# Kernel tuning notes

Measured on AMD Instinct MI355X. Metric: run time of the kernel, lower is better.

The kernel has to match this reference:

```python
import jax, jax.numpy as jnp
import numpy as np
import math

D_MODEL, D_K, D_V, H = 512, 64, 64, 8

def setup_inputs() -> dict:
    key = jax.random.key(0)
    ks = jax.random.split(key, 8)
    B, L = 2, 4096
    q = jax.random.normal(ks[0], (B, L, D_MODEL), dtype=jnp.float32)
    k = jax.random.normal(ks[1], (B, L, D_MODEL), dtype=jnp.float32)
    v = jax.random.normal(ks[2], (B, L, D_MODEL), dtype=jnp.float32)
    attention_mask = jnp.ones((B, L), dtype=jnp.int32)
    s = 1.0 / math.sqrt(D_MODEL)
    Wq = jax.random.uniform(ks[3], (D_MODEL, H * D_K), dtype=jnp.float32, minval=-s, maxval=s)
    Wk = jax.random.uniform(ks[4], (D_MODEL, H * D_K), dtype=jnp.float32, minval=-s, maxval=s)
    Wv = jax.random.uniform(ks[5], (D_MODEL, H * D_V), dtype=jnp.float32, minval=-s, maxval=s)
    so = 1.0 / math.sqrt(H * D_V)
    Wo = jax.random.uniform(ks[6], (H * D_V, D_MODEL), dtype=jnp.float32, minval=-so, maxval=so)
    return {"q": q, "k": k, "v": v, "attention_mask": attention_mask,
            "Wq": Wq, "Wk": Wk, "Wv": Wv, "Wo": Wo}

def reference(q, k, v, attention_mask, Wq, Wk, Wv, Wo):
    B, L, _ = q.shape
    scale = 1.0 / math.sqrt(D_K)
    # project and split heads: [B, H, L, d]
    qh = (q @ Wq).reshape(B, L, H, D_K).transpose(0, 2, 1, 3)
    kh = (k @ Wk).reshape(B, L, H, D_K).transpose(0, 2, 1, 3)
    vh = (v @ Wv).reshape(B, L, H, D_V).transpose(0, 2, 1, 3)
    score = jnp.einsum('bhqd,bhkd->bhqk', qh, kh) * scale  # [B,H,L,L]
    mask = attention_mask[:, None, None, :]  # [B,1,1,L]
    score = jnp.where(mask == 0, -jnp.inf, score)
    attn = jax.nn.softmax(score, axis=-1)
    out = jnp.einsum('bhqk,bhkd->bhqd', attn, vh)
    out = out.transpose(0, 2, 1, 3).reshape(B, L, H * D_V)
    return out @ Wo
```

## Files before the change

kernel.cpp:

```cpp
#include <hip/hip_runtime.h>

typedef short bf16x8 __attribute__((ext_vector_type(8)));
typedef float f32x4 __attribute__((ext_vector_type(4)));
typedef unsigned short u16x8 __attribute__((ext_vector_type(8)));

static __device__ __forceinline__ unsigned short f2bf(float f) {
  unsigned int x = __builtin_bit_cast(unsigned int, f);
  x += 0x7FFFu + ((x >> 16) & 1u);
  return (unsigned short)(x >> 16);
}
static __device__ __forceinline__ unsigned int pk2bf(float a, float b) {
  unsigned int ia = __builtin_bit_cast(unsigned int, a) + 0x8000u;
  unsigned int ib = __builtin_bit_cast(unsigned int, b) + 0x8000u;
  return __builtin_amdgcn_perm(ib, ia, 0x07060302u);
}
static __device__ __forceinline__ void gl2lds16(const unsigned short* g, unsigned short* l) {
  __builtin_amdgcn_global_load_lds(
      (const __attribute__((address_space(1))) unsigned int*)g,
      (__attribute__((address_space(3))) unsigned int*)l, 16, 0, 0);
}

__global__ __launch_bounds__(256) void cvt3(const float* __restrict__ q, const float* __restrict__ k,
                                            const float* __restrict__ v,
                                            unsigned short* __restrict__ xbf) {
  const int sec = blockIdx.y;
  const float* src = (sec == 0) ? q : (sec == 1) ? k : v;
  int i = (blockIdx.x * 256 + threadIdx.x) * 8;
  int row = i >> 9, col = i & 511;
  float4 a = *(const float4*)(src + i);
  float4 b = *(const float4*)(src + i + 4);
  uint4 pk;
  pk.x = pk2bf(a.x, a.y); pk.y = pk2bf(a.z, a.w);
  pk.z = pk2bf(b.x, b.y); pk.w = pk2bf(b.z, b.w);
  *(uint4*)(xbf + (size_t)row * 1536 + sec * 512 + col) = pk;
}

__global__ __launch_bounds__(256) void wtrans4(const float* __restrict__ Wq, const float* __restrict__ Wk,
                                               const float* __restrict__ Wv, const float* __restrict__ Wo,
                                               unsigned short* __restrict__ WT) {
  __shared__ __align__(16) float T[64 * 68];
  const int z = blockIdx.z;
  const float* W = (z == 0) ? Wq : (z == 1) ? Wk : (z == 2) ? Wv : Wo;
  unsigned short* out = WT + (size_t)z * 512 * 512;
  const int k0 = blockIdx.x * 64, n0 = blockIdx.y * 64;
  const int tid = threadIdx.x;
#pragma unroll
  for (int i = 0; i < 4; ++i) {
    int chunk = i * 256 + tid;
    int row = chunk >> 4, fc = chunk & 15;
    *(float4*)(T + row * 68 + fc * 4) =
        *(const float4*)(W + (size_t)(k0 + row) * 512 + n0 + fc * 4);
  }
  __syncthreads();
#pragma unroll
  for (int i = 0; i < 2; ++i) {
    int chunk = i * 256 + tid;
    int nr = chunk >> 3, kc = chunk & 7;
    u16x8 v;
#pragma unroll
    for (int j = 0; j < 8; ++j) v[j] = f2bf(T[(kc * 8 + j) * 68 + nr]);
    *(u16x8*)(out + (size_t)(n0 + nr) * 512 + k0 + kc * 8) = v;
  }
}

__global__ __launch_bounds__(256) void gemm_qkv(const unsigned short* __restrict__ xbf,
                                                const unsigned short* __restrict__ Bt,
                                                unsigned short* __restrict__ C,
                                                float qscale) {
  __shared__ __align__(16) unsigned short Abuf[2][128 * 32];
  __shared__ __align__(16) unsigned short Bbuf[2][128 * 32];
  const int by = blockIdx.y;
  const unsigned short* A = xbf + (by >> 2) * 512;
  const float scale = (by < 4) ? qscale : 1.0f;
  const int tid = threadIdx.x;
  const int wid = tid >> 6, lane = tid & 63, quad = lane >> 4, li = lane & 15;
  const int bm = blockIdx.x * 128, bn = by * 128;
  const int wm = (wid & 1) * 64, wn = (wid >> 1) * 64;
  const unsigned short* ga[2]; int oa[2];
  const unsigned short* gb[2]; int obx[2];
#pragma unroll
  for (int i = 0; i < 2; ++i) {
    int lam = i * 256 + tid;
    int r = lam >> 2, c = (lam & 3) ^ (r & 3);
    ga[i] = A + (size_t)(bm + r) * 1536 + c * 8;
    oa[i] = lam * 8;
    gb[i] = Bt + (size_t)(bn + r) * 512 + c * 8;
    obx[i] = lam * 8;
  }
#pragma unroll
  for (int i = 0; i < 2; ++i) {
    gl2lds16(ga[i], &Abuf[0][oa[i]]); ga[i] += 32;
    gl2lds16(gb[i], &Bbuf[0][obx[i]]); gb[i] += 32;
  }
  f32x4 acc[4][4] = {};
  const int sw = li & 3;
  for (int s = 0; s < 16; ++s) {
    __syncthreads();
    if (s + 1 < 16) {
      int p = (s + 1) & 1;
#pragma unroll
      for (int i = 0; i < 2; ++i) {
        gl2lds16(ga[i], &Abuf[p][oa[i]]); ga[i] += 32;
        gl2lds16(gb[i], &Bbuf[p][obx[i]]); gb[i] += 32;
      }
    }
    const unsigned short* As = &Abuf[s & 1][0];
    const unsigned short* Bs = &Bbuf[s & 1][0];
    bf16x8 af[4], bfr[4];
#pragma unroll
    for (int t = 0; t < 4; ++t) {
      af[t]  = *(const bf16x8*)(As + (wm + t * 16 + li) * 32 + ((quad ^ sw) * 8));
      bfr[t] = *(const bf16x8*)(Bs + (wn + t * 16 + li) * 32 + ((quad ^ sw) * 8));
    }
#pragma unroll
    for (int mt = 0; mt < 4; ++mt)
#pragma unroll
      for (int nt = 0; nt < 4; ++nt)
        acc[mt][nt] = __builtin_amdgcn_mfma_f32_16x16x32_bf16(af[mt], bfr[nt], acc[mt][nt], 0, 0, 0);
  }
#pragma unroll
  for (int mt = 0; mt < 4; ++mt)
#pragma unroll
    for (int nt = 0; nt < 4; ++nt) {
      int r0 = bm + wm + mt * 16 + quad * 4;
      int c  = bn + wn + nt * 16 + li;
#pragma unroll
      for (int r = 0; r < 4; ++r)
        C[(size_t)(r0 + r) * 1536 + c] = f2bf(acc[mt][nt][r] * scale);
    }
}

__global__ __launch_bounds__(256) void gemm_o(const unsigned short* __restrict__ A,
                                              const unsigned short* __restrict__ Bt,
                                              float* __restrict__ Cf) {
  __shared__ __align__(16) unsigned short Abuf[2][128 * 64];
  __shared__ __align__(16) unsigned short Bbuf[2][64 * 64];
  const int K = 512, LDC = 512;
  const int tid = threadIdx.x;
  const int wid = tid >> 6, lane = tid & 63, quad = lane >> 4, li = lane & 15;
  const int bm = blockIdx.x * 128, bn = blockIdx.y * 64;
  const int wm = wid * 32;
  const unsigned short* ga[4]; int oa[4];
  const unsigned short* gb[2]; int ob[2];
#pragma unroll
  for (int i = 0; i < 4; ++i) {
    int lam = i * 256 + wid * 64 + lane;
    int r = lam >> 3, c = (lam & 7) ^ (r & 7);
    ga[i] = A + (size_t)(bm + r) * K + c * 8;
    oa[i] = lam * 8;
  }
#pragma unroll
  for (int i = 0; i < 2; ++i) {
    int lam = i * 256 + wid * 64 + lane;
    int r = lam >> 3, c = (lam & 7) ^ (r & 7);
    gb[i] = Bt + (size_t)(bn + r) * K + c * 8;
    ob[i] = lam * 8;
  }
#pragma unroll
  for (int i = 0; i < 4; ++i) { gl2lds16(ga[i], &Abuf[0][oa[i]]); ga[i] += 64; }
#pragma unroll
  for (int i = 0; i < 2; ++i) { gl2lds16(gb[i], &Bbuf[0][ob[i]]); gb[i] += 64; }

  f32x4 acc[2][4] = {};
  const int sw = li & 7;
  for (int s = 0; s < 8; ++s) {
    __syncthreads();
    if (s + 1 < 8) {
      int p = (s + 1) & 1;
#pragma unroll
      for (int i = 0; i < 4; ++i) { gl2lds16(ga[i], &Abuf[p][oa[i]]); ga[i] += 64; }
#pragma unroll
      for (int i = 0; i < 2; ++i) { gl2lds16(gb[i], &Bbuf[p][ob[i]]); gb[i] += 64; }
    }
    const unsigned short* As = &Abuf[s & 1][0];
    const unsigned short* Bs = &Bbuf[s & 1][0];
#pragma unroll
    for (int kk = 0; kk < 2; ++kk) {
      bf16x8 af[2], bfr[4];
#pragma unroll
      for (int t = 0; t < 2; ++t)
        af[t] = *(const bf16x8*)(As + (wm + t * 16 + li) * 64 + (((kk * 4 + quad) ^ sw) * 8));
#pragma unroll
      for (int t = 0; t < 4; ++t)
        bfr[t] = *(const bf16x8*)(Bs + (t * 16 + li) * 64 + (((kk * 4 + quad) ^ sw) * 8));
#pragma unroll
      for (int mt = 0; mt < 2; ++mt)
#pragma unroll
        for (int nt = 0; nt < 4; ++nt)
          acc[mt][nt] = __builtin_amdgcn_mfma_f32_16x16x32_bf16(af[mt], bfr[nt], acc[mt][nt], 0, 0, 0);
    }
  }
#pragma unroll
  for (int mt = 0; mt < 2; ++mt)
#pragma unroll
    for (int nt = 0; nt < 4; ++nt) {
      int r0 = bm + wm + mt * 16 + quad * 4;
      int c  = bn + nt * 16 + li;
#pragma unroll
      for (int r = 0; r < 4; ++r)
        Cf[(size_t)(r0 + r) * LDC + c] = acc[mt][nt][r];
    }
}

__global__ __launch_bounds__(256) void vtrans(const unsigned short* __restrict__ qkv,
                                              unsigned short* __restrict__ vt) {
  __shared__ __align__(16) unsigned short T[64 * 72];
  const int kt = blockIdx.x;
  const int bh = blockIdx.y;
  const int b = bh >> 3, h = bh & 7;
  const int tid = threadIdx.x;
#pragma unroll
  for (int i = 0; i < 2; ++i) {
    int chunk = i * 256 + tid;
    int row = chunk >> 3, c8 = chunk & 7;
    *(uint4*)(T + row * 72 + c8 * 8) =
        *(const uint4*)(qkv + (size_t)(b * 4096 + kt * 64 + row) * 1536 + 1024 + h * 64 + c8 * 8);
  }
  __syncthreads();
#pragma unroll
  for (int i = 0; i < 2; ++i) {
    int chunk = i * 256 + tid;
    int dr = chunk >> 3, c8 = chunk & 7;
    u16x8 v;
#pragma unroll
    for (int j = 0; j < 8; ++j) v[j] = T[(c8 * 8 + j) * 72 + dr];
    *(u16x8*)(vt + (size_t)(bh * 64 + dr) * 4096 + kt * 64 + c8 * 8) = v;
  }
}

__global__ __launch_bounds__(512) void attn(const unsigned short* __restrict__ qkv,
                                            const unsigned short* __restrict__ vt,
                                            const int* __restrict__ mask,
                                            float* __restrict__ O0, float* __restrict__ O1,
                                            float* __restrict__ Lb) {
  __shared__ __align__(16) unsigned short Kbuf[2][64 * 64];
  __shared__ __align__(16) unsigned short Vbuf[2][64 * 64];
  __shared__ __align__(16) unsigned short Psh[8][32 * 72];
  __shared__ __align__(16) unsigned short MskBits[256];
  const int qt = blockIdx.x, h = blockIdx.y, z = blockIdx.z;
  const int b = z >> 1, half = z & 1;
  const int t0 = half * 32;
  const int tid = threadIdx.x;
  const int wid = tid >> 6, lane = tid & 63, quad = lane >> 4, li = lane & 15;
  const size_t tok0 = (size_t)b * 4096;

  if (tid < 256) {
    const int4* mp = (const int4*)(mask + b * 4096 + tid * 16);
    unsigned int bits = 0;
#pragma unroll
    for (int j = 0; j < 4; ++j) {
      int4 m4 = mp[j];
      bits |= (m4.x ? 1u : 0u) << (j * 4 + 0);
      bits |= (m4.y ? 1u : 0u) << (j * 4 + 1);
      bits |= (m4.z ? 1u : 0u) << (j * 4 + 2);
      bits |= (m4.w ? 1u : 0u) << (j * 4 + 3);
    }
    MskBits[tid] = (unsigned short)bits;
  }

  const unsigned short* qpa = qkv + (tok0 + qt * 256 + wid * 32 + li) * 1536 + h * 64;
  const unsigned short* qpb = qpa + 16 * 1536;
  bf16x8 bq0a = *(const bf16x8*)(qpa + quad * 8);
  bf16x8 bq1a = *(const bf16x8*)(qpa + 32 + quad * 8);
  bf16x8 bq0b = *(const bf16x8*)(qpb + quad * 8);
  bf16x8 bq1b = *(const bf16x8*)(qpb + 32 + quad * 8);

  const unsigned short* kbase = qkv + tok0 * 1536 + 512 + h * 64;
  const unsigned short* vbase = vt + (size_t)(b * 8 + h) * 64 * 4096;
  const int wk = wid & 3;
  const int lam0 = wk * 128 + lane, lam1 = lam0 + 64;
  const int r0 = lam0 >> 3, c0 = (lam0 & 7) ^ (r0 & 7);
  const int r1 = lam1 >> 3, c1 = (lam1 & 7) ^ (r1 & 7);
  const unsigned short *g0, *g1;
  size_t kstride;
  unsigned short *lb0, *lb1;
  if (wid < 4) {
    g0 = kbase + (size_t)(t0 * 64 + r0) * 1536 + c0 * 8;
    g1 = kbase + (size_t)(t0 * 64 + r1) * 1536 + c1 * 8;
    kstride = (size_t)64 * 1536;
    lb0 = &Kbuf[0][0]; lb1 = &Kbuf[1][0];
  } else {
    g0 = vbase + (size_t)r0 * 4096 + t0 * 64 + c0 * 8;
    g1 = vbase + (size_t)r1 * 4096 + t0 * 64 + c1 * 8;
    kstride = 64;
    lb0 = &Vbuf[0][0]; lb1 = &Vbuf[1][0];
  }
  const int o0 = lam0 * 8, o1 = lam1 * 8;

  gl2lds16(g0, lb0 + o0);
  gl2lds16(g1, lb0 + o1);
  g0 += kstride; g1 += kstride;

  f32x4 accOa[4] = {}, accOb[4] = {};
  f32x4 accLa = {}, accLb = {};
  bf16x8 bones;
#pragma unroll
  for (int j = 0; j < 8; ++j) bones[j] = (short)0x3F80;
  unsigned short* Pw = &Psh[wid][0];
  const int sw = li & 7;

  for (int tt = 0; tt < 32; ++tt) {
    const int t = t0 + tt;
    __syncthreads();
    if (tt < 31) {
      unsigned short* lb = ((tt + 1) & 1) ? lb1 : lb0;
      gl2lds16(g0, lb + o0);
      gl2lds16(g1, lb + o1);
      g0 += kstride; g1 += kstride;
    }
    const unsigned short* Ks = &Kbuf[tt & 1][0];
    const unsigned short* Vs = &Vbuf[tt & 1][0];

    f32x4 sa[4], sb[4];
#pragma unroll
    for (int kb = 0; kb < 4; ++kb) {
      const unsigned short* kr = Ks + (kb * 16 + li) * 64;
      bf16x8 ak0 = *(const bf16x8*)(kr + ((quad ^ sw) * 8));
      bf16x8 ak1 = *(const bf16x8*)(kr + (((4 + quad) ^ sw) * 8));
      f32x4 za = {}, zb = {};
      za = __builtin_amdgcn_mfma_f32_16x16x32_bf16(ak0, bq0a, za, 0, 0, 0);
      za = __builtin_amdgcn_mfma_f32_16x16x32_bf16(ak1, bq1a, za, 0, 0, 0);
      zb = __builtin_amdgcn_mfma_f32_16x16x32_bf16(ak0, bq0b, zb, 0, 0, 0);
      zb = __builtin_amdgcn_mfma_f32_16x16x32_bf16(ak1, bq1b, zb, 0, 0, 0);
      sa[kb] = za; sb[kb] = zb;
    }
    unsigned long long mbits = *(const unsigned long long*)(MskBits + t * 4);
    if (mbits != ~0ull) {
#pragma unroll
      for (int kb = 0; kb < 4; ++kb)
#pragma unroll
        for (int r = 0; r < 4; ++r) {
          int key = kb * 16 + quad * 4 + r;
          if (!((mbits >> key) & 1ull)) { sa[kb][r] = -1e30f; sb[kb][r] = -1e30f; }
        }
    }
#pragma unroll
    for (int kb = 0; kb < 4; ++kb) {
#pragma unroll
      for (int r = 0; r < 4; ++r) {
        sa[kb][r] = __builtin_amdgcn_exp2f(sa[kb][r]);
        sb[kb][r] = __builtin_amdgcn_exp2f(sb[kb][r]);
      }
      uint2 pka, pkb;
      pka.x = pk2bf(sa[kb][0], sa[kb][1]); pka.y = pk2bf(sa[kb][2], sa[kb][3]);
      pkb.x = pk2bf(sb[kb][0], sb[kb][1]); pkb.y = pk2bf(sb[kb][2], sb[kb][3]);
      *(uint2*)(Pw + li * 72 + kb * 16 + quad * 4) = pka;
      *(uint2*)(Pw + (li + 16) * 72 + kb * 16 + quad * 4) = pkb;
    }
    bf16x8 p0a = *(const bf16x8*)(Pw + li * 72 + quad * 8);
    bf16x8 p1a = *(const bf16x8*)(Pw + li * 72 + 32 + quad * 8);
    bf16x8 p0b = *(const bf16x8*)(Pw + (li + 16) * 72 + quad * 8);
    bf16x8 p1b = *(const bf16x8*)(Pw + (li + 16) * 72 + 32 + quad * 8);
#pragma unroll
    for (int dc = 0; dc < 4; ++dc) {
      const unsigned short* vr = Vs + (dc * 16 + li) * 64;
      bf16x8 bv0 = *(const bf16x8*)(vr + ((quad ^ sw) * 8));
      bf16x8 bv1 = *(const bf16x8*)(vr + (((4 + quad) ^ sw) * 8));
      accOa[dc] = __builtin_amdgcn_mfma_f32_16x16x32_bf16(p0a, bv0, accOa[dc], 0, 0, 0);
      accOa[dc] = __builtin_amdgcn_mfma_f32_16x16x32_bf16(p1a, bv1, accOa[dc], 0, 0, 0);
      accOb[dc] = __builtin_amdgcn_mfma_f32_16x16x32_bf16(p0b, bv0, accOb[dc], 0, 0, 0);
      accOb[dc] = __builtin_amdgcn_mfma_f32_16x16x32_bf16(p1b, bv1, accOb[dc], 0, 0, 0);
    }
    accLa = __builtin_amdgcn_mfma_f32_16x16x32_bf16(p0a, bones, accLa, 0, 0, 0);
    accLa = __builtin_amdgcn_mfma_f32_16x16x32_bf16(p1a, bones, accLa, 0, 0, 0);
    accLb = __builtin_amdgcn_mfma_f32_16x16x32_bf16(p0b, bones, accLb, 0, 0, 0);
    accLb = __builtin_amdgcn_mfma_f32_16x16x32_bf16(p1b, bones, accLb, 0, 0, 0);
  }
  float* Oh = half ? O1 : O0;
  const size_t rqa = tok0 + qt * 256 + wid * 32 + quad * 4;
  const size_t rqb = rqa + 16;
#pragma unroll
  for (int dc = 0; dc < 4; ++dc) {
    size_t col = h * 64 + dc * 16 + li;
#pragma unroll
    for (int r = 0; r < 4; ++r) {
      Oh[(rqa + r) * 512 + col] = accOa[dc][r];
      Oh[(rqb + r) * 512 + col] = accOb[dc][r];
    }
  }
  if (li == 0) {
#pragma unroll
    for (int r = 0; r < 4; ++r) {
      Lb[((size_t)half * 8192 + rqa + r) * 8 + h] = accLa[r];
      Lb[((size_t)half * 8192 + rqb + r) * 8 + h] = accLb[r];
    }
  }
}

__global__ __launch_bounds__(256) void cmb(const float* __restrict__ O0, const float* __restrict__ O1,
                                           const float* __restrict__ Lb,
                                           unsigned short* __restrict__ ob) {
  int idx = (blockIdx.x * 256 + threadIdx.x) * 4;
  int tok = idx >> 9, h = (idx >> 6) & 7;
  float inv = 1.f / (Lb[(size_t)tok * 8 + h] + Lb[(size_t)(8192 + tok) * 8 + h]);
  float4 a = *(const float4*)(O0 + idx);
  float4 b = *(const float4*)(O1 + idx);
  uint2 pk;
  pk.x = pk2bf((a.x + b.x) * inv, (a.y + b.y) * inv);
  pk.y = pk2bf((a.z + b.z) * inv, (a.w + b.w) * inv);
  *(uint2*)(ob + idx) = pk;
}

extern "C" void kernel_launch(void* const* d_in, const int* in_sizes, int n_in,
                              void* d_out, int out_size, void* d_ws, size_t ws_size,
                              hipStream_t stream) {
  const float* q  = (const float*)d_in[0];
  const float* k  = (const float*)d_in[1];
  const float* v  = (const float*)d_in[2];
  const int* mask = (const int*)d_in[3];
  const float* Wq = (const float*)d_in[4];
  const float* Wk = (const float*)d_in[5];
  const float* Wv = (const float*)d_in[6];
  const float* Wo = (const float*)d_in[7];
  float* out = (float*)d_out;

  char* ws = (char*)d_ws;
  const size_t MB = 1024 * 1024;
  unsigned short* xbf  = (unsigned short*)(ws);
  unsigned short* vtb  = (unsigned short*)(ws + 16 * MB);
  unsigned short* obb  = (unsigned short*)(ws + 16 * MB);
  unsigned short* qkvh = (unsigned short*)(ws + 24 * MB);
  unsigned short* wAll = (unsigned short*)(ws + 48 * MB);
  unsigned short* woT  = wAll + (size_t)3 * 512 * 512;
  float* O0f = (float*)(ws);
  float* O1f = (float*)(ws + 50 * MB);
  float* Lb  = (float*)(ws + 66 * MB);

  dim3 cg(2048, 3);
  cvt3<<<cg, 256, 0, stream>>>(q, k, v, xbf);
  dim3 wg(8, 8, 4);
  wtrans4<<<wg, 256, 0, stream>>>(Wq, Wk, Wv, Wo, wAll);
  const float qscale = 0.125f * 1.44269504f;
  dim3 gq(64, 12);
  gemm_qkv<<<gq, 256, 0, stream>>>(xbf, wAll, qkvh, qscale);
  dim3 vg(64, 16);
  vtrans<<<vg, 256, 0, stream>>>(qkvh, vtb);
  dim3 ag(16, 8, 4);
  attn<<<ag, 512, 0, stream>>>(qkvh, vtb, mask, O0f, O1f, Lb);
  cmb<<<4096, 256, 0, stream>>>(O0f, O1f, Lb, obb);
  dim3 go(64, 8);
  gemm_o<<<go, 256, 0, stream>>>(obb, woT, out);
}
```

Baseline: 232.4 us.

## Pre-pack K/V into MFMA fragment layout and drop LDS staging in attention

A new kvfrag kernel rewrites K and V into per-tile MFMA fragment order, so the attention kernel loads its operands straight from global memory into registers. This removes the LDS double buffering and the per-iteration block barriers. The input conversion and weight transpose kernels are also merged into one launch. In exchange, every wave now reads K/V fragments from global or L2 on its own instead of sharing one LDS copy per block, so global traffic goes up and load latency is no longer hidden by the barrier-synchronised prefetch.

```diff
diff --git a/kernel.cpp b/kernel.cpp
--- a/kernel.cpp
+++ b/kernel.cpp
@@ -20,46 +20,49 @@
       (__attribute__((address_space(3))) unsigned int*)l, 16, 0, 0);
 }
 
-__global__ __launch_bounds__(256) void cvt3(const float* __restrict__ q, const float* __restrict__ k,
+__global__ __launch_bounds__(256) void prep(const float* __restrict__ q, const float* __restrict__ k,
                                             const float* __restrict__ v,
-                                            unsigned short* __restrict__ xbf) {
-  const int sec = blockIdx.y;
-  const float* src = (sec == 0) ? q : (sec == 1) ? k : v;
-  int i = (blockIdx.x * 256 + threadIdx.x) * 8;
-  int row = i >> 9, col = i & 511;
-  float4 a = *(const float4*)(src + i);
-  float4 b = *(const float4*)(src + i + 4);
-  uint4 pk;
-  pk.x = pk2bf(a.x, a.y); pk.y = pk2bf(a.z, a.w);
-  pk.z = pk2bf(b.x, b.y); pk.w = pk2bf(b.z, b.w);
-  *(uint4*)(xbf + (size_t)row * 1536 + sec * 512 + col) = pk;
-}
-
-__global__ __launch_bounds__(256) void wtrans4(const float* __restrict__ Wq, const float* __restrict__ Wk,
-                                               const float* __restrict__ Wv, const float* __restrict__ Wo,
-                                               unsigned short* __restrict__ WT) {
+                                            const float* __restrict__ Wq, const float* __restrict__ Wk,
+                                            const float* __restrict__ Wv, const float* __restrict__ Wo,
+                                            unsigned short* __restrict__ xbf,
+                                            unsigned short* __restrict__ WT) {
   __shared__ __align__(16) float T[64 * 68];
-  const int z = blockIdx.z;
-  const float* W = (z == 0) ? Wq : (z == 1) ? Wk : (z == 2) ? Wv : Wo;
-  unsigned short* out = WT + (size_t)z * 512 * 512;
-  const int k0 = blockIdx.x * 64, n0 = blockIdx.y * 64;
+  const int bid = blockIdx.x;
   const int tid = threadIdx.x;
-#pragma unroll
-  for (int i = 0; i < 4; ++i) {
-    int chunk = i * 256 + tid;
-    int row = chunk >> 4, fc = chunk & 15;
-    *(float4*)(T + row * 68 + fc * 4) =
-        *(const float4*)(W + (size_t)(k0 + row) * 512 + n0 + fc * 4);
-  }
-  __syncthreads();
-#pragma unroll
-  for (int i = 0; i < 2; ++i) {
-    int chunk = i * 256 + tid;
-    int nr = chunk >> 3, kc = chunk & 7;
-    u16x8 v;
-#pragma unroll
-    for (int j = 0; j < 8; ++j) v[j] = f2bf(T[(kc * 8 + j) * 68 + nr]);
-    *(u16x8*)(out + (size_t)(n0 + nr) * 512 + k0 + kc * 8) = v;
+  if (bid < 6144) {
+    const int sec = bid / 2048;
+    const float* src = (sec == 0) ? q : (sec == 1) ? k : v;
+    int i = ((bid % 2048) * 256 + tid) * 8;
+    int row = i >> 9, col = i & 511;
+    float4 a = *(const float4*)(src + i);
+    float4 b = *(const float4*)(src + i + 4);
+    uint4 pk;
+    pk.x = pk2bf(a.x, a.y); pk.y = pk2bf(a.z, a.w);
+    pk.z = pk2bf(b.x, b.y); pk.w = pk2bf(b.z, b.w);
+    *(uint4*)(xbf + (size_t)row * 1536 + sec * 512 + col) = pk;
+  } else {
+    const int w = bid - 6144;
+    const int z = w >> 6;
+    const float* W = (z == 0) ? Wq : (z == 1) ? Wk : (z == 2) ? Wv : Wo;
+    unsigned short* out = WT + (size_t)z * 512 * 512;
+    const int k0 = ((w >> 3) & 7) * 64, n0 = (w & 7) * 64;
+#pragma unroll
+    for (int i = 0; i < 4; ++i) {
+      int chunk = i * 256 + tid;
+      int row = chunk >> 4, fc = chunk & 15;
+      *(float4*)(T + row * 68 + fc * 4) =
+          *(const float4*)(W + (size_t)(k0 + row) * 512 + n0 + fc * 4);
+    }
+    __syncthreads();
+#pragma unroll
+    for (int i = 0; i < 2; ++i) {
+      int chunk = i * 256 + tid;
+      int nr = chunk >> 3, kc = chunk & 7;
+      u16x8 vv;
+#pragma unroll
+      for (int j = 0; j < 8; ++j) vv[j] = f2bf(T[(kc * 8 + j) * 68 + nr]);
+      *(u16x8*)(out + (size_t)(n0 + nr) * 512 + k0 + kc * 8) = vv;
+    }
   }
 }
 
@@ -130,6 +133,179 @@
     }
 }
 
+__global__ __launch_bounds__(512) void kvfrag(const unsigned short* __restrict__ qkv,
+                                              unsigned short* __restrict__ kfr,
+                                              unsigned short* __restrict__ vfr) {
+  __shared__ __align__(16) unsigned short Ksh[64 * 72];
+  __shared__ __align__(16) unsigned short Vsh[64 * 72];
+  const int kt = blockIdx.x, bh = blockIdx.y;
+  const int b = bh >> 3, h = bh & 7;
+  const int tid = threadIdx.x;
+  {
+    int row = tid >> 3, c8 = tid & 7;
+    const unsigned short* src = qkv + (size_t)(b * 4096 + kt * 64 + row) * 1536 + h * 64 + c8 * 8;
+    *(uint4*)(Ksh + row * 72 + c8 * 8) = *(const uint4*)(src + 512);
+    *(uint4*)(Vsh + row * 72 + c8 * 8) = *(const uint4*)(src + 1024);
+  }
+  __syncthreads();
+  const int fi = tid >> 6, l = tid & 63;
+  const size_t obase = ((size_t)(bh * 64 + kt) * 8 + fi) * 512 + l * 8;
+  {
+    int kb = fi >> 1, dh = fi & 1;
+    uint4 kf = *(const uint4*)(Ksh + (kb * 16 + (l & 15)) * 72 + (l >> 4) * 8 + dh * 32);
+    *(uint4*)(kfr + obase) = kf;
+  }
+  {
+    int dc = fi >> 1, kh = fi & 1;
+    u16x8 vf;
+#pragma unroll
+    for (int j = 0; j < 8; ++j)
+      vf[j] = Vsh[((l >> 4) * 8 + kh * 32 + j) * 72 + dc * 16 + (l & 15)];
+    *(u16x8*)(vfr + obase) = vf;
+  }
+}
+
+__global__ __launch_bounds__(512, 4) void attn(const unsigned short* __restrict__ qkv,
+                                               const unsigned short* __restrict__ kfr,
+                                               const unsigned short* __restrict__ vfr,
+                                               const int* __restrict__ mask,
+                                               float* __restrict__ O0, float* __restrict__ O1,
+                                               float* __restrict__ Lb) {
+  __shared__ __align__(16) unsigned short Psh[8][32 * 72];
+  __shared__ __align__(16) unsigned short MskBits[256];
+  const int qt = blockIdx.x, h = blockIdx.y, z = blockIdx.z;
+  const int b = z >> 1, half = z & 1;
+  const int t0 = half * 32;
+  const int tid = threadIdx.x;
+  const int wid = tid >> 6, lane = tid & 63, quad = lane >> 4, li = lane & 15;
+  const size_t tok0 = (size_t)b * 4096;
+  const int bh = b * 8 + h;
+
+  if (tid < 256) {
+    const int4* mp = (const int4*)(mask + b * 4096 + tid * 16);
+    unsigned int bits = 0;
+#pragma unroll
+    for (int j = 0; j < 4; ++j) {
+      int4 m4 = mp[j];
+      bits |= (m4.x ? 1u : 0u) << (j * 4 + 0);
+      bits |= (m4.y ? 1u : 0u) << (j * 4 + 1);
+      bits |= (m4.z ? 1u : 0u) << (j * 4 + 2);
+      bits |= (m4.w ? 1u : 0u) << (j * 4 + 3);
+    }
+    MskBits[tid] = (unsigned short)bits;
+  }
+  __syncthreads();
+
+  const unsigned short* qpa = qkv + (tok0 + qt * 256 + wid * 32 + li) * 1536 + h * 64;
+  const unsigned short* qpb = qpa + 16 * 1536;
+  bf16x8 bq0a = *(const bf16x8*)(qpa + quad * 8);
+  bf16x8 bq1a = *(const bf16x8*)(qpa + 32 + quad * 8);
+  bf16x8 bq0b = *(const bf16x8*)(qpb + quad * 8);
+  bf16x8 bq1b = *(const bf16x8*)(qpb + 32 + quad * 8);
+
+  const unsigned short* kbp = kfr + ((size_t)(bh * 64 + t0) * 8) * 512 + lane * 8;
+  const unsigned short* vbp = vfr + ((size_t)(bh * 64 + t0) * 8) * 512 + lane * 8;
+
+  f32x4 accOa[4] = {}, accOb[4] = {};
+  f32x4 accLa = {}, accLb = {};
+  bf16x8 bones;
+#pragma unroll
+  for (int j = 0; j < 8; ++j) bones[j] = (short)0x3F80;
+  unsigned short* Pw = &Psh[wid][0];
+
+  for (int tt = 0; tt < 32; ++tt) {
+    const int t = t0 + tt;
+    bf16x8 kf[8];
+#pragma unroll
+    for (int fi = 0; fi < 8; ++fi) kf[fi] = *(const bf16x8*)(kbp + fi * 512);
+    f32x4 sa[4], sb[4];
+#pragma unroll
+    for (int kb = 0; kb < 4; ++kb) {
+      f32x4 za = {}, zb = {};
+      za = __builtin_amdgcn_mfma_f32_16x16x32_bf16(kf[kb * 2], bq0a, za, 0, 0, 0);
+      za = __builtin_amdgcn_mfma_f32_16x16x32_bf16(kf[kb * 2 + 1], bq1a, za, 0, 0, 0);
+      zb = __builtin_amdgcn_mfma_f32_16x16x32_bf16(kf[kb * 2], bq0b, zb, 0, 0, 0);
+      zb = __builtin_amdgcn_mfma_f32_16x16x32_bf16(kf[kb * 2 + 1], bq1b, zb, 0, 0, 0);
+      sa[kb] = za; sb[kb] = zb;
+    }
+    unsigned long long mbits = *(const unsigned long long*)(MskBits + t * 4);
+    if (mbits != ~0ull) {
+#pragma unroll
+      for (int kb = 0; kb < 4; ++kb)
+#pragma unroll
+        for (int r = 0; r < 4; ++r) {
+          int key = kb * 16 + quad * 4 + r;
+          if (!((mbits >> key) & 1ull)) { sa[kb][r] = -1e30f; sb[kb][r] = -1e30f; }
+        }
+    }
+#pragma unroll
+    for (int kb = 0; kb < 4; ++kb) {
+#pragma unroll
+      for (int r = 0; r < 4; ++r) {
+        sa[kb][r] = __builtin_amdgcn_exp2f(sa[kb][r]);
+        sb[kb][r] = __builtin_amdgcn_exp2f(sb[kb][r]);
+      }
+      uint2 pka, pkb;
+      pka.x = pk2bf(sa[kb][0], sa[kb][1]); pka.y = pk2bf(sa[kb][2], sa[kb][3]);
+      pkb.x = pk2bf(sb[kb][0], sb[kb][1]); pkb.y = pk2bf(sb[kb][2], sb[kb][3]);
+      *(uint2*)(Pw + li * 72 + kb * 16 + quad * 4) = pka;
+      *(uint2*)(Pw + (li + 16) * 72 + kb * 16 + quad * 4) = pkb;
+    }
+    bf16x8 p0a = *(const bf16x8*)(Pw + li * 72 + quad * 8);
+    bf16x8 p1a = *(const bf16x8*)(Pw + li * 72 + 32 + quad * 8);
+    bf16x8 p0b = *(const bf16x8*)(Pw + (li + 16) * 72 + quad * 8);
+    bf16x8 p1b = *(const bf16x8*)(Pw + (li + 16) * 72 + 32 + quad * 8);
+#pragma unroll
+    for (int dc = 0; dc < 4; ++dc) {
+      bf16x8 bv0 = *(const bf16x8*)(vbp + (dc * 2) * 512);
+      bf16x8 bv1 = *(const bf16x8*)(vbp + (dc * 2 + 1) * 512);
+      accOa[dc] = __builtin_amdgcn_mfma_f32_16x16x32_bf16(p0a, bv0, accOa[dc], 0, 0, 0);
+      accOa[dc] = __builtin_amdgcn_mfma_f32_16x16x32_bf16(p1a, bv1, accOa[dc], 0, 0, 0);
+      accOb[dc] = __builtin_amdgcn_mfma_f32_16x16x32_bf16(p0b, bv0, accOb[dc], 0, 0, 0);
+      accOb[dc] = __builtin_amdgcn_mfma_f32_16x16x32_bf16(p1b, bv1, accOb[dc], 0, 0, 0);
+    }
+    accLa = __builtin_amdgcn_mfma_f32_16x16x32_bf16(p0a, bones, accLa, 0, 0, 0);
+    accLa = __builtin_amdgcn_mfma_f32_16x16x32_bf16(p1a, bones, accLa, 0, 0, 0);
+    accLb = __builtin_amdgcn_mfma_f32_16x16x32_bf16(p0b, bones, accLb, 0, 0, 0);
+    accLb = __builtin_amdgcn_mfma_f32_16x16x32_bf16(p1b, bones, accLb, 0, 0, 0);
+    kbp += 8 * 512;
+    vbp += 8 * 512;
+  }
+  float* Oh = half ? O1 : O0;
+  const size_t rqa = tok0 + qt * 256 + wid * 32 + quad * 4;
+  const size_t rqb = rqa + 16;
+#pragma unroll
+  for (int dc = 0; dc < 4; ++dc) {
+    size_t col = h * 64 + dc * 16 + li;
+#pragma unroll
+    for (int r = 0; r < 4; ++r) {
+      Oh[(rqa + r) * 512 + col] = accOa[dc][r];
+      Oh[(rqb + r) * 512 + col] = accOb[dc][r];
+    }
+  }
+  if (li == 0) {
+#pragma unroll
+    for (int r = 0; r < 4; ++r) {
+      Lb[((size_t)half * 8192 + rqa + r) * 8 + h] = accLa[r];
+      Lb[((size_t)half * 8192 + rqb + r) * 8 + h] = accLb[r];
+    }
+  }
+}
+
+__global__ __launch_bounds__(256) void cmb(const float* __restrict__ O0, const float* __restrict__ O1,
+                                           const float* __restrict__ Lb,
+                                           unsigned short* __restrict__ ob) {
+  int idx = (blockIdx.x * 256 + threadIdx.x) * 4;
+  int tok = idx >> 9, h = (idx >> 6) & 7;
+  float inv = 1.f / (Lb[(size_t)tok * 8 + h] + Lb[(size_t)(8192 + tok) * 8 + h]);
+  float4 a = *(const float4*)(O0 + idx);
+  float4 b = *(const float4*)(O1 + idx);
+  uint2 pk;
+  pk.x = pk2bf((a.x + b.x) * inv, (a.y + b.y) * inv);
+  pk.y = pk2bf((a.z + b.z) * inv, (a.w + b.w) * inv);
+  *(uint2*)(ob + idx) = pk;
+}
+
 __global__ __launch_bounds__(256) void gemm_o(const unsigned short* __restrict__ A,
                                               const unsigned short* __restrict__ Bt,
                                               float* __restrict__ Cf) {
@@ -202,205 +378,6 @@
     }
 }
 
-__global__ __launch_bounds__(256) void vtrans(const unsigned short* __restrict__ qkv,
-                                              unsigned short* __restrict__ vt) {
-  __shared__ __align__(16) unsigned short T[64 * 72];
-  const int kt = blockIdx.x;
-  const int bh = blockIdx.y;
-  const int b = bh >> 3, h = bh & 7;
-  const int tid = threadIdx.x;
-#pragma unroll
-  for (int i = 0; i < 2; ++i) {
-    int chunk = i * 256 + tid;
-    int row = chunk >> 3, c8 = chunk & 7;
-    *(uint4*)(T + row * 72 + c8 * 8) =
-        *(const uint4*)(qkv + (size_t)(b * 4096 + kt * 64 + row) * 1536 + 1024 + h * 64 + c8 * 8);
-  }
-  __syncthreads();
-#pragma unroll
-  for (int i = 0; i < 2; ++i) {
-    int chunk = i * 256 + tid;
-    int dr = chunk >> 3, c8 = chunk & 7;
-    u16x8 v;
-#pragma unroll
-    for (int j = 0; j < 8; ++j) v[j] = T[(c8 * 8 + j) * 72 + dr];
-    *(u16x8*)(vt + (size_t)(bh * 64 + dr) * 4096 + kt * 64 + c8 * 8) = v;
-  }
-}
-
-__global__ __launch_bounds__(512) void attn(const unsigned short* __restrict__ qkv,
-                                            const unsigned short* __restrict__ vt,
-                                            const int* __restrict__ mask,
-                                            float* __restrict__ O0, float* __restrict__ O1,
-                                            float* __restrict__ Lb) {
-  __shared__ __align__(16) unsigned short Kbuf[2][64 * 64];
-  __shared__ __align__(16) unsigned short Vbuf[2][64 * 64];
-  __shared__ __align__(16) unsigned short Psh[8][32 * 72];
-  __shared__ __align__(16) unsigned short MskBits[256];
-  const int qt = blockIdx.x, h = blockIdx.y, z = blockIdx.z;
-  const int b = z >> 1, half = z & 1;
-  const int t0 = half * 32;
-  const int tid = threadIdx.x;
-  const int wid = tid >> 6, lane = tid & 63, quad = lane >> 4, li = lane & 15;
-  const size_t tok0 = (size_t)b * 4096;
-
-  if (tid < 256) {
-    const int4* mp = (const int4*)(mask + b * 4096 + tid * 16);
-    unsigned int bits = 0;
-#pragma unroll
-    for (int j = 0; j < 4; ++j) {
-      int4 m4 = mp[j];
-      bits |= (m4.x ? 1u : 0u) << (j * 4 + 0);
-      bits |= (m4.y ? 1u : 0u) << (j * 4 + 1);
-      bits |= (m4.z ? 1u : 0u) << (j * 4 + 2);
-      bits |= (m4.w ? 1u : 0u) << (j * 4 + 3);
-    }
-    MskBits[tid] = (unsigned short)bits;
-  }
-
-  const unsigned short* qpa = qkv + (tok0 + qt * 256 + wid * 32 + li) * 1536 + h * 64;
-  const unsigned short* qpb = qpa + 16 * 1536;
-  bf16x8 bq0a = *(const bf16x8*)(qpa + quad * 8);
-  bf16x8 bq1a = *(const bf16x8*)(qpa + 32 + quad * 8);
-  bf16x8 bq0b = *(const bf16x8*)(qpb + quad * 8);
-  bf16x8 bq1b = *(const bf16x8*)(qpb + 32 + quad * 8);
-
-  const unsigned short* kbase = qkv + tok0 * 1536 + 512 + h * 64;
-  const unsigned short* vbase = vt + (size_t)(b * 8 + h) * 64 * 4096;
-  const int wk = wid & 3;
-  const int lam0 = wk * 128 + lane, lam1 = lam0 + 64;
-  const int r0 = lam0 >> 3, c0 = (lam0 & 7) ^ (r0 & 7);
-  const int r1 = lam1 >> 3, c1 = (lam1 & 7) ^ (r1 & 7);
-  const unsigned short *g0, *g1;
-  size_t kstride;
-  unsigned short *lb0, *lb1;
-  if (wid < 4) {
-    g0 = kbase + (size_t)(t0 * 64 + r0) * 1536 + c0 * 8;
-    g1 = kbase + (size_t)(t0 * 64 + r1) * 1536 + c1 * 8;
-    kstride = (size_t)64 * 1536;
-    lb0 = &Kbuf[0][0]; lb1 = &Kbuf[1][0];
-  } else {
-    g0 = vbase + (size_t)r0 * 4096 + t0 * 64 + c0 * 8;
-    g1 = vbase + (size_t)r1 * 4096 + t0 * 64 + c1 * 8;
-    kstride = 64;
-    lb0 = &Vbuf[0][0]; lb1 = &Vbuf[1][0];
-  }
-  const int o0 = lam0 * 8, o1 = lam1 * 8;
-
-  gl2lds16(g0, lb0 + o0);
-  gl2lds16(g1, lb0 + o1);
-  g0 += kstride; g1 += kstride;
-
-  f32x4 accOa[4] = {}, accOb[4] = {};
-  f32x4 accLa = {}, accLb = {};
-  bf16x8 bones;
-#pragma unroll
-  for (int j = 0; j < 8; ++j) bones[j] = (short)0x3F80;
-  unsigned short* Pw = &Psh[wid][0];
-  const int sw = li & 7;
-
-  for (int tt = 0; tt < 32; ++tt) {
-    const int t = t0 + tt;
-    __syncthreads();
-    if (tt < 31) {
-      unsigned short* lb = ((tt + 1) & 1) ? lb1 : lb0;
-      gl2lds16(g0, lb + o0);
-      gl2lds16(g1, lb + o1);
-      g0 += kstride; g1 += kstride;
-    }
-    const unsigned short* Ks = &Kbuf[tt & 1][0];
-    const unsigned short* Vs = &Vbuf[tt & 1][0];
-
-    f32x4 sa[4], sb[4];
-#pragma unroll
-    for (int kb = 0; kb < 4; ++kb) {
-      const unsigned short* kr = Ks + (kb * 16 + li) * 64;
-      bf16x8 ak0 = *(const bf16x8*)(kr + ((quad ^ sw) * 8));
-      bf16x8 ak1 = *(const bf16x8*)(kr + (((4 + quad) ^ sw) * 8));
-      f32x4 za = {}, zb = {};
-      za = __builtin_amdgcn_mfma_f32_16x16x32_bf16(ak0, bq0a, za, 0, 0, 0);
-      za = __builtin_amdgcn_mfma_f32_16x16x32_bf16(ak1, bq1a, za, 0, 0, 0);
-      zb = __builtin_amdgcn_mfma_f32_16x16x32_bf16(ak0, bq0b, zb, 0, 0, 0);
-      zb = __builtin_amdgcn_mfma_f32_16x16x32_bf16(ak1, bq1b, zb, 0, 0, 0);
-      sa[kb] = za; sb[kb] = zb;
-    }
-    unsigned long long mbits = *(const unsigned long long*)(MskBits + t * 4);
-    if (mbits != ~0ull) {
-#pragma unroll
-      for (int kb = 0; kb < 4; ++kb)
-#pragma unroll
-        for (int r = 0; r < 4; ++r) {
-          int key = kb * 16 + quad * 4 + r;
-          if (!((mbits >> key) & 1ull)) { sa[kb][r] = -1e30f; sb[kb][r] = -1e30f; }
-        }
-    }
-#pragma unroll
-    for (int kb = 0; kb < 4; ++kb) {
-#pragma unroll
-      for (int r = 0; r < 4; ++r) {
-        sa[kb][r] = __builtin_amdgcn_exp2f(sa[kb][r]);
-        sb[kb][r] = __builtin_amdgcn_exp2f(sb[kb][r]);
-      }
-      uint2 pka, pkb;
-      pka.x = pk2bf(sa[kb][0], sa[kb][1]); pka.y = pk2bf(sa[kb][2], sa[kb][3]);
-      pkb.x = pk2bf(sb[kb][0], sb[kb][1]); pkb.y = pk2bf(sb[kb][2], sb[kb][3]);
-      *(uint2*)(Pw + li * 72 + kb * 16 + quad * 4) = pka;
-      *(uint2*)(Pw + (li + 16) * 72 + kb * 16 + quad * 4) = pkb;
-    }
-    bf16x8 p0a = *(const bf16x8*)(Pw + li * 72 + quad * 8);
-    bf16x8 p1a = *(const bf16x8*)(Pw + li * 72 + 32 + quad * 8);
-    bf16x8 p0b = *(const bf16x8*)(Pw + (li + 16) * 72 + quad * 8);
-    bf16x8 p1b = *(const bf16x8*)(Pw + (li + 16) * 72 + 32 + quad * 8);
-#pragma unroll
-    for (int dc = 0; dc < 4; ++dc) {
-      const unsigned short* vr = Vs + (dc * 16 + li) * 64;
-      bf16x8 bv0 = *(const bf16x8*)(vr + ((quad ^ sw) * 8));
-      bf16x8 bv1 = *(const bf16x8*)(vr + (((4 + quad) ^ sw) * 8));
-      accOa[dc] = __builtin_amdgcn_mfma_f32_16x16x32_bf16(p0a, bv0, accOa[dc], 0, 0, 0);
-      accOa[dc] = __builtin_amdgcn_mfma_f32_16x16x32_bf16(p1a, bv1, accOa[dc], 0, 0, 0);
-      accOb[dc] = __builtin_amdgcn_mfma_f32_16x16x32_bf16(p0b, bv0, accOb[dc], 0, 0, 0);
-      accOb[dc] = __builtin_amdgcn_mfma_f32_16x16x32_bf16(p1b, bv1, accOb[dc], 0, 0, 0);
-    }
-    accLa = __builtin_amdgcn_mfma_f32_16x16x32_bf16(p0a, bones, accLa, 0, 0, 0);
-    accLa = __builtin_amdgcn_mfma_f32_16x16x32_bf16(p1a, bones, accLa, 0, 0, 0);
-    accLb = __builtin_amdgcn_mfma_f32_16x16x32_bf16(p0b, bones, accLb, 0, 0, 0);
-    accLb = __builtin_amdgcn_mfma_f32_16x16x32_bf16(p1b, bones, accLb, 0, 0, 0);
-  }
-  float* Oh = half ? O1 : O0;
-  const size_t rqa = tok0 + qt * 256 + wid * 32 + quad * 4;
-  const size_t rqb = rqa + 16;
-#pragma unroll
-  for (int dc = 0; dc < 4; ++dc) {
-    size_t col = h * 64 + dc * 16 + li;
-#pragma unroll
-    for (int r = 0; r < 4; ++r) {
-      Oh[(rqa + r) * 512 + col] = accOa[dc][r];
-      Oh[(rqb + r) * 512 + col] = accOb[dc][r];
-    }
-  }
-  if (li == 0) {
-#pragma unroll
-    for (int r = 0; r < 4; ++r) {
-      Lb[((size_t)half * 8192 + rqa + r) * 8 + h] = accLa[r];
-      Lb[((size_t)half * 8192 + rqb + r) * 8 + h] = accLb[r];
-    }
-  }
-}
-
-__global__ __launch_bounds__(256) void cmb(const float* __restrict__ O0, const float* __restrict__ O1,
-                                           const float* __restrict__ Lb,
-                                           unsigned short* __restrict__ ob) {
-  int idx = (blockIdx.x * 256 + threadIdx.x) * 4;
-  int tok = idx >> 9, h = (idx >> 6) & 7;
-  float inv = 1.f / (Lb[(size_t)tok * 8 + h] + Lb[(size_t)(8192 + tok) * 8 + h]);
-  float4 a = *(const float4*)(O0 + idx);
-  float4 b = *(const float4*)(O1 + idx);
-  uint2 pk;
-  pk.x = pk2bf((a.x + b.x) * inv, (a.y + b.y) * inv);
-  pk.y = pk2bf((a.z + b.z) * inv, (a.w + b.w) * inv);
-  *(uint2*)(ob + idx) = pk;
-}
-
 extern "C" void kernel_launch(void* const* d_in, const int* in_sizes, int n_in,
                               void* d_out, int out_size, void* d_ws, size_t ws_size,
                               hipStream_t stream) {
@@ -416,27 +393,25 @@
 
   char* ws = (char*)d_ws;
   const size_t MB = 1024 * 1024;
-  unsigned short* xbf  = (unsigned short*)(ws);
-  unsigned short* vtb  = (unsigned short*)(ws + 16 * MB);
-  unsigned short* obb  = (unsigned short*)(ws + 16 * MB);
-  unsigned short* qkvh = (unsigned short*)(ws + 24 * MB);
-  unsigned short* wAll = (unsigned short*)(ws + 48 * MB);
+  unsigned short* kfr  = (unsigned short*)(ws);
+  unsigned short* vfr  = (unsigned short*)(ws + 16 * MB);
+  unsigned short* qkvh = (unsigned short*)(ws + 32 * MB);
+  unsigned short* xbf  = (unsigned short*)(ws + 56 * MB);
+  float* O0f = (float*)(ws + 56 * MB);
+  float* O1f = (float*)(ws + 72 * MB);
+  float* Lb  = (float*)(ws + 88 * MB);
+  unsigned short* wAll = (unsigned short*)(ws + 89 * MB);
   unsigned short* woT  = wAll + (size_t)3 * 512 * 512;
-  float* O0f = (float*)(ws);
-  float* O1f = (float*)(ws + 50 * MB);
-  float* Lb  = (float*)(ws + 66 * MB);
-
-  dim3 cg(2048, 3);
-  cvt3<<<cg, 256, 0, stream>>>(q, k, v, xbf);
-  dim3 wg(8, 8, 4);
-  wtrans4<<<wg, 256, 0, stream>>>(Wq, Wk, Wv, Wo, wAll);
+  unsigned short* obb  = (unsigned short*)(ws);
+
+  prep<<<6400, 256, 0, stream>>>(q, k, v, Wq, Wk, Wv, Wo, xbf, wAll);
   const float qscale = 0.125f * 1.44269504f;
   dim3 gq(64, 12);
   gemm_qkv<<<gq, 256, 0, stream>>>(xbf, wAll, qkvh, qscale);
-  dim3 vg(64, 16);
-  vtrans<<<vg, 256, 0, stream>>>(qkvh, vtb);
+  dim3 fg(64, 16);
+  kvfrag<<<fg, 512, 0, stream>>>(qkvh, kfr, vfr);
   dim3 ag(16, 8, 4);
-  attn<<<ag, 512, 0, stream>>>(qkvh, vtb, mask, O0f, O1f, Lb);
+  attn<<<ag, 512, 0, stream>>>(qkvh, kfr, vfr, mask, O0f, O1f, Lb);
   cmb<<<4096, 256, 0, stream>>>(O0f, O1f, Lb, obb);
   dim3 go(64, 8);
   gemm_o<<<go, 256, 0, stream>>>(obb, woT, out);
```

Measured after the change: 237.4 us. 1.02x slower.
